# Optimization experiments

Hardware: AMD Instinct MI355X
Metric: run time of the kernel (lower is better)

Reference implementation:

```python
import math
import jax, jax.numpy as jnp
from jax import lax
import numpy as np

B, T_ENC, T_DEC = 32, 256, 800
ENC_SPK, POS_D, MAX_LEN = 896, 128, 100
N_MEL, PRE, ATT, DEC = 80, 256, 1024, 1024
IN1 = PRE + ENC_SPK + POS_D  # 1280 = first_rnn input
PROJ_IN = DEC + ENC_SPK + POS_D  # 2048


def make_pe(max_len, d):
    pe = np.zeros((max_len, d), np.float32)
    pos = np.arange(max_len, dtype=np.float32)[:, None]
    div = np.exp(np.arange(0, d, 2, dtype=np.float32) * (-math.log(10000.0) / d))
    pe[:, 0::2] = np.sin(pos * div)
    pe[:, 1::2] = np.cos(pos * div)
    return jnp.asarray(pe)


def lstm_cell(x, h, c, W_ih, W_hh, b_ih, b_hh):
    g = x @ W_ih.T + b_ih + h @ W_hh.T + b_hh
    i, f, gg, o = jnp.split(g, 4, axis=-1)  # torch LSTMCell gate order i,f,g,o
    c_new = jax.nn.sigmoid(f) * c + jax.nn.sigmoid(i) * jnp.tanh(gg)
    h_new = jax.nn.sigmoid(o) * jnp.tanh(c_new)
    return h_new, c_new


def setup_inputs() -> dict:
    key = jax.random.key(0)
    ks = jax.random.split(key, 24)
    s = 0.02  # weight init scale
    inp = {}
    inp["memory"] = jax.random.normal(ks[0], (B, T_ENC, ENC_SPK), jnp.float32)
    inp["durations_in_frames"] = jax.random.uniform(ks[1], (B, T_ENC), jnp.float32, 1.0, 7.0)
    inp["duration_frames_indices"] = jax.random.randint(ks[2], (B, T_DEC), 0, MAX_LEN)
    inp["range_pred"] = jax.random.uniform(ks[3], (B, T_ENC, 1), jnp.float32, 0.5, 2.5)
    inp["decoder_inputs"] = jax.random.normal(ks[4], (B, N_MEL, T_DEC), jnp.float32)
    inp["memory_lengths"] = jax.random.randint(ks[5], (B,), T_ENC // 2, T_ENC + 1)
    # prenet (no bias)
    inp["W_p1"] = jax.random.normal(ks[6], (PRE, N_MEL), jnp.float32) * s
    inp["W_p2"] = jax.random.normal(ks[7], (PRE, PRE), jnp.float32) * s
    # first LSTMCell
    inp["W_ih1"] = jax.random.normal(ks[8], (4 * ATT, IN1), jnp.float32) * s
    inp["W_hh1"] = jax.random.normal(ks[9], (4 * ATT, ATT), jnp.float32) * s
    inp["b_ih1"] = jnp.zeros((4 * ATT,), jnp.float32)
    inp["b_hh1"] = jnp.zeros((4 * ATT,), jnp.float32)
    # second LSTMCell
    inp["W_ih2"] = jax.random.normal(ks[10], (4 * DEC, ATT), jnp.float32) * s
    inp["W_hh2"] = jax.random.normal(ks[11], (4 * DEC, DEC), jnp.float32) * s
    inp["b_ih2"] = jnp.zeros((4 * DEC,), jnp.float32)
    inp["b_hh2"] = jnp.zeros((4 * DEC,), jnp.float32)
    # linear projection (2048 -> 80)
    inp["W_proj"] = jax.random.normal(ks[12], (N_MEL, PROJ_IN), jnp.float32) * s
    inp["b_proj"] = jnp.zeros((N_MEL,), jnp.float32)
    # deterministic prenet dropout uniforms (p=0.5, training=True always in Prenet)
    inp["u1"] = jax.random.uniform(ks[13], (T_DEC + 1, B, PRE), jnp.float32)
    inp["u2"] = jax.random.uniform(ks[14], (T_DEC + 1, B, PRE), jnp.float32)
    return inp


def reference(memory, durations_in_frames, duration_frames_indices, range_pred,
              decoder_inputs, memory_lengths,
              W_p1, W_p2, W_ih1, W_hh1, b_ih1, b_hh1,
              W_ih2, W_hh2, b_ih2, b_hh2, W_proj, b_proj, u1, u2):
    dtype = memory.dtype
    pe = make_pe(MAX_LEN, POS_D)
    # parse decoder inputs: [B, n_mel, T] -> [T, B, n_mel]; prepend go frame
    dec_in = jnp.transpose(decoder_inputs, (2, 0, 1))
    dec_in = jnp.concatenate([jnp.zeros((1, B, N_MEL), dtype), dec_in], axis=0)
    # prenet: relu->dropout(0.5) x2 (inverted dropout, scale 1/(1-p)=2)
    m1 = jnp.where(u1 >= 0.5, 2.0, 0.0).astype(dtype)
    m2 = jnp.where(u2 >= 0.5, 2.0, 0.0).astype(dtype)
    x = jax.nn.relu(dec_in @ W_p1.T) * m1
    x = jax.nn.relu(x @ W_p2.T) * m2  # [T_DEC+1, B, PRE]
    prenet_out = x[:T_DEC]
    # Gaussian upsampling constants (independent of decoder step)
    sigma = range_pred[..., 0] + 1e-05                      # [B, T_ENC]
    c_vec = jnp.cumsum(durations_in_frames, axis=1) - durations_in_frames / 2
    coef = 1.0 / jnp.sqrt(2.0 * np.pi * sigma ** 2)
    steps = jnp.arange(T_DEC, dtype=dtype)
    pos_t = duration_frames_indices.T                       # [T_DEC, B]

    def step(carry, inp):
        h1, c1, h2, c2 = carry
        x_t, t, pos = inp
        prob = coef * jnp.exp(-((t - c_vec) ** 2) / (sigma ** 2) / 2) + 1e-05
        w = prob / jnp.sum(prob, axis=1, keepdims=True)     # [B, T_ENC]
        ctx = jnp.einsum('bt,bte->be', w, memory)           # [B, ENC_SPK]
        ctx_pe = jnp.concatenate([ctx, pe[pos]], axis=-1)   # [B, ENC_SPK+POS_D]
        inp1 = jnp.concatenate([x_t, ctx_pe], axis=-1)
        h1, c1 = lstm_cell(inp1, h1, c1, W_ih1, W_hh1, b_ih1, b_hh1)
        h2, c2 = lstm_cell(h1, h2, c2, W_ih2, W_hh2, b_ih2, b_hh2)
        mel = jnp.concatenate([h2, ctx_pe], axis=1) @ W_proj.T + b_proj
        return (h1, c1, h2, c2), (mel, w)

    init = (jnp.zeros((B, ATT), dtype), jnp.zeros((B, ATT), dtype),
            jnp.zeros((B, DEC), dtype), jnp.zeros((B, DEC), dtype))
    _, (mels, ws) = lax.scan(step, init, (prenet_out, steps, pos_t))
    mel_outputs = jnp.transpose(mels, (1, 2, 0))            # [B, N_MEL, T_DEC]
    alignments = jnp.transpose(ws, (1, 0, 2))               # [B, T_DEC, T_ENC]
    return mel_outputs, alignments
```

## Files before the change

kernel.cpp:

```cpp
#include <hip/hip_runtime.h>
#include <hip/hip_bf16.h>
#include <math.h>

typedef __attribute__((ext_vector_type(8))) short bfrag8;
typedef __attribute__((ext_vector_type(4))) float f32x4;
#define AGENT __HIP_MEMORY_SCOPE_AGENT

static __device__ __forceinline__ float b2f(unsigned short u) {
  union { unsigned int i; float f; } v; v.i = ((unsigned int)u) << 16; return v.f;
}
static __device__ __forceinline__ unsigned short f2b(float f) {
  union { float f; unsigned int i; } v; v.f = f;
  unsigned int i = v.i;
  return (unsigned short)((i + 0x7FFFu + ((i >> 16) & 1u)) >> 16);
}
static __device__ __forceinline__ float sigf(float x) { return 1.f / (1.f + __expf(-x)); }


__global__ void k_init(unsigned int* hzero, unsigned int* cnt, float* pe) {
  int idx = blockIdx.x * 256 + threadIdx.x;
  if (idx < 256) cnt[idx] = 0u;
  if (idx < 65536) hzero[idx] = 0u;
  if (idx < 6400) {
    int p = idx >> 6, i = idx & 63;
// ... 74 lines not shown
  float p = coef[b * 256 + e] * __expf(-dt * dt * inv2[b * 256 + e]) + 1e-5f;
  float s = p;
#pragma unroll
  for (int o = 1; o < 64; o <<= 1) s += __shfl_xor(s, o);
  if ((e & 63) == 0) red[e >> 6] = s;
  __syncthreads();
  float tot = red[0] + red[1] + red[2] + red[3];
  out_align[((size_t)b * 800 + t) * 256 + e] = p / tot;
}

__global__ __launch_bounds__(256) void k_ctx(const float* __restrict__ cvec,
                                             const float* __restrict__ coef,
                                             const float* __restrict__ inv2,
                                             const float* __restrict__ mem,
                                             unsigned short* inp1c,
                                             int t0, int tbeg, int tend) {
  __shared__ float wl[4096];
  __shared__ float rinv[16];
  int b = blockIdx.y, tB = tbeg + blockIdx.x * 16, tid = threadIdx.x;
  int nt = tend - tB; if (nt > 16) nt = 16;
  float cv = cvec[b * 256 + tid], co = coef[b * 256 + tid], iv = inv2[b * 256 + tid];
  for (int s = 0; s < nt; ++s) {
    float d = (float)(tB + s) - cv;
    wl[s * 256 + tid] = co * __expf(-d * d * iv) + 1e-5f;
  }
  for (int s = nt; s < 16; ++s) wl[s * 256 + tid] = 0.f;
  __syncthreads();
  int wv = tid >> 6, ln = tid & 63;
  for (int s = wv; s < nt; s += 4) {
    float x = wl[s * 256 + ln] + wl[s * 256 + 64 + ln] + wl[s * 256 + 128 + ln] + wl[s * 256 + 192 + ln];
#pragma unroll
    for (int o = 1; o < 64; o <<= 1) x += __shfl_xor(x, o);
    if (ln == 0) rinv[s] = 1.f / x;
  }
  __syncthreads();
  for (int s = 0; s < nt; ++s) wl[s * 256 + tid] *= rinv[s];
  __syncthreads();
  float acc[16][4];
#pragma unroll
  for (int s = 0; s < 16; ++s) { acc[s][0] = 0.f; acc[s][1] = 0.f; acc[s][2] = 0.f; acc[s][3] = 0.f; }
  for (int e = 0; e < 256; ++e) {
    const float* mrow = mem + ((size_t)b * 256 + e) * 896;
    float m0 = mrow[tid], m1 = mrow[tid + 256], m2 = mrow[tid + 512];
    float m3 = (tid < 128) ? mrow[tid + 768] : 0.f;
#pragma unroll
    for (int s = 0; s < 16; ++s) {
      float w = wl[s * 256 + e];
      acc[s][0] += w * m0; acc[s][1] += w * m1; acc[s][2] += w * m2; acc[s][3] += w * m3;
    }
  }
  for (int s = 0; s < nt; ++s) {
    size_t base = ((size_t)(tB - t0 + s) * 32 + b) * 1280 + 256;
    inp1c[base + tid]       = f2b(acc[s][0]);
    inp1c[base + tid + 256] = f2b(acc[s][1]);
    inp1c[base + tid + 512] = f2b(acc[s][2]);
    if (tid < 128) inp1c[base + tid + 768] = f2b(acc[s][3]);
  }
}

__global__ void k_pegather(const int* __restrict__ dfi, const float* __restrict__ pe,
                           unsigned short* inp1c, int t0, int tbeg, int R) {
  int idx = blockIdx.x * 256 + threadIdx.x;
  if (idx >= R * 4096) return;
  int d = idx & 127, r = idx >> 7;
  int b = r & 31, ti = r >> 5;
  int t = tbeg + ti;
  int pos = dfi[b * 800 + t];
  inp1c[((size_t)(t - t0) * 32 + b) * 1280 + 1152 + d] = f2b(pe[pos * 128 + d]);
}

__global__ void k_repackW(const float* __restrict__ Wih1, unsigned short* wbf) {
  int idx = blockIdx.x * 256 + threadIdx.x;
  if (idx >= 1310720) return;
  float4 f = *(const float4*)(Wih1 + (size_t)idx * 4);
  union { unsigned short us[4]; unsigned long long q; } o;
  o.us[0] = f2b(f.x); o.us[1] = f2b(f.y); o.us[2] = f2b(f.z); o.us[3] = f2b(f.w);
  *(unsigned long long*)(wbf + (size_t)idx * 4) = o.q;
}

__global__ void k_repackImg(const float* __restrict__ Whh1, const float* __restrict__ Wih2,
                            const float* __restrict__ Whh2, unsigned short* wimg) {
  size_t idx = (size_t)blockIdx.x * 256 + threadIdx.x;
  if (idx >= 12582912ull) return;
  int wg = (int)(idx / 49152);
  int rem = (int)(idx % 49152);
  int gi = rem / 16384;
  int r2 = rem & 16383;
  int ks = r2 >> 9;
  int l  = (r2 >> 3) & 63;
  int e  = r2 & 7;
  int nn = l & 15, kq = l >> 4;
  int row = (nn >> 2) * 1024 + wg * 4 + (nn & 3);
  int kk = ks * 32 + kq * 8 + e;
  const float* W = (gi == 0) ? Whh1 : (gi == 1) ? Wih2 : Whh2;
  wimg[idx] = f2b(W[(size_t)row * 1024 + kk]);
}

__global__ __launch_bounds__(256) void k_melpre(const unsigned short* __restrict__ inp1c,
                                                const float* __restrict__ Wproj,
                                                const float* __restrict__ bproj,
                                                unsigned short* melpre, int t0, int tbeg) {
  extern __shared__ unsigned short ctx[];
  int t = tbeg + blockIdx.x, tid = threadIdx.x;
  int tt = t - t0;
  for (int i = tid; i < 32768; i += 256)
    ctx[i] = inp1c[((size_t)tt * 32 + (i >> 10)) * 1280 + 256 + (i & 1023)];
  __syncthreads();
  if (tid < 240) {
    int c = tid % 80, bs = tid / 80;
    const float* w = Wproj + (size_t)c * 2048 + 1024;
    for (int b = bs; b < 32; b += 3) {
      float s = bproj[c];
      const unsigned short* x = ctx + b * 1024;
#pragma unroll 8
      for (int kk = 0; kk < 1024; ++kk) s += b2f(x[kk]) * w[kk];
      melpre[((size_t)t * 32 + b) * 80 + c] = f2b(s);
    }
  }
}

#define COH_LOAD8(d0,d1,d2,d3,d4,d5,d6,d7, p0,p1,p2,p3,p4,p5,p6,p7)       \
  asm volatile(                                                            \
    "global_load_dwordx4 %0, %8, off sc0 sc1\n\t"                          \
    "global_load_dwordx4 %1, %9, off sc0 sc1\n\t"                          \
    "global_load_dwordx4 %2, %10, off sc0 sc1\n\t"                         \
    "global_load_dwordx4 %3, %11, off sc0 sc1\n\t"                         \
    "global_load_dwordx4 %4, %12, off sc0 sc1\n\t"                         \
    "global_load_dwordx4 %5, %13, off sc0 sc1\n\t"                         \
    "global_load_dwordx4 %6, %14, off sc0 sc1\n\t"                         \
    "global_load_dwordx4 %7, %15, off sc0 sc1\n\t"                         \
    "s_waitcnt vmcnt(0)"                                                   \
    : "=&v"(d0), "=&v"(d1), "=&v"(d2), "=&v"(d3),                          \
      "=&v"(d4), "=&v"(d5), "=&v"(d6), "=&v"(d7)                           \
    : "v"(p0), "v"(p1), "v"(p2), "v"(p3),                                  \
      "v"(p4), "v"(p5), "v"(p6), "v"(p7)                                   \
    : "memory")

struct DecArgs {
  const unsigned short* inp1c;
  const unsigned short* wbf;
  const unsigned short* wimg;
  const float* bih1; const float* bhh1; const float* bih2; const float* bhh2;
  const float* Wproj; const float* bproj;
  const unsigned short* melpre;
  unsigned short* h1; unsigned short* h2; float* cst;
  unsigned int* cnt; float* out_mel;
  int k0, k1;
};

__global__ __launch_bounds__(512, 1) void k_decode(DecArgs A) {
  extern __shared__ char smem[];
  float (*g1)[17]  = (float(*)[17])(smem + 131072);
  float (*g2a)[17] = (float(*)[17])(smem + 133248);
  float (*g2b)[17] = (float(*)[17])(smem + 135424);
  float (*c1)[4]   = (float(*)[4])(smem + 137600);
  float (*c2)[4]   = (float(*)[4])(smem + 138112);
  float* bias1     = (float*)(smem + 138624);
  float* bias2     = (float*)(smem + 138688);

  int wg = blockIdx.x, tid = threadIdx.x;
  int wid = tid >> 6, lane = tid & 63;
  int k0 = A.k0, k1 = A.k1;
  const unsigned short* wimg_wg = A.wimg + (size_t)wg * 49152;

  if (tid < 16) {
    int row = (tid >> 2) * 1024 + wg * 4 + (tid & 3);
    bias1[tid] = A.bih1[row] + A.bhh1[row];
    bias2[tid] = A.bih2[row] + A.bhh2[row];
  }
  if (tid < 128) {
    int b = tid >> 2, jj = tid & 3;
    c1[b][jj] = (k0 == 0) ? 0.f : A.cst[((size_t)wg * 32 + b) * 4 + jj];
  } else if (tid < 256) {
    int b = (tid - 128) >> 2, jj = tid & 3;
    c2[b][jj] = (k0 == 0) ? 0.f : A.cst[32768 + ((size_t)wg * 32 + b) * 4 + jj];
  }
  __syncthreads();

  long totspin = 0;
  for (int k = k0; k < k1; ++k) {
    bool do1 = (k < 800);
    bool do2 = (k >= 1 && k <= 800);

    {
      const char* s1 = (const char*)(A.h1 + ((k - 1) & 1) * 32768);
      const char* s2 = (const char*)(A.h2 + (k & 1) * 32768);
      ulonglong2 d0,d1,d2,d3,d4,d5,d6,d7, e0,e1,e2,e3,e4,e5,e6,e7;
      COH_LOAD8(d0,d1,d2,d3,d4,d5,d6,d7,
                s1 + ((size_t)(0*512)+tid)*16, s1 + ((size_t)(1*512)+tid)*16,
                s1 + ((size_t)(2*512)+tid)*16, s1 + ((size_t)(3*512)+tid)*16,
                s1 + ((size_t)(4*512)+tid)*16, s1 + ((size_t)(5*512)+tid)*16,
                s1 + ((size_t)(6*512)+tid)*16, s1 + ((size_t)(7*512)+tid)*16);
      COH_LOAD8(e0,e1,e2,e3,e4,e5,e6,e7,
                s2 + ((size_t)(0*512)+tid)*16, s2 + ((size_t)(1*512)+tid)*16,
                s2 + ((size_t)(2*512)+tid)*16, s2 + ((size_t)(3*512)+tid)*16,
                s2 + ((size_t)(4*512)+tid)*16, s2 + ((size_t)(5*512)+tid)*16,
                s2 + ((size_t)(6*512)+tid)*16, s2 + ((size_t)(7*512)+tid)*16);
#define STG_WR(j, va, vb)                                            \
      { int m = (j)*512 + tid;                                       \
        int sw = (m * 16) ^ (((m >> 7) & 7) << 4);                   \
        *(ulonglong2*)(smem + sw) = va;                              \
        *(ulonglong2*)(smem + 65536 + sw) = vb; }
      STG_WR(0, d0, e0); STG_WR(1, d1, e1); STG_WR(2, d2, e2); STG_WR(3, d3, e3);
      STG_WR(4, d4, e4); STG_WR(5, d5, e5); STG_WR(6, d6, e6); STG_WR(7, d7, e7);
#undef STG_WR
    }
    __syncthreads();

    if (wid < 2) {
      if (do1) {
        int nn = lane & 15, kq = lane >> 4;
        int brow = wid * 16 + nn;
        int row = (nn >> 2) * 1024 + wg * 4 + (nn & 3);
        f32x4 a0 = {0.f,0.f,0.f,0.f}, a1 = {0.f,0.f,0.f,0.f};
        size_t tt = (size_t)(k - k0 + 2);
        const unsigned short* arow = A.inp1c + (tt * 32 + brow) * 1280 + kq * 8;
        const unsigned short* wrow = A.wbf + (size_t)row * 1280 + kq * 8;
#pragma unroll 4
        for (int ks = 0; ks < 40; ks += 2) {
          bfrag8 aA = *(const bfrag8*)(arow + ks * 32);
          bfrag8 aB = *(const bfrag8*)(arow + ks * 32 + 32);
          bfrag8 b0 = *(const bfrag8*)(wrow + ks * 32);
          bfrag8 b1 = *(const bfrag8*)(wrow + ks * 32 + 32);
          a0 = __builtin_amdgcn_mfma_f32_16x16x32_bf16(aA, b0, a0, 0, 0, 0);
          a1 = __builtin_amdgcn_mfma_f32_16x16x32_bf16(aB, b1, a1, 0, 0, 0);
        }
        const bfrag8* bp = (const bfrag8*)wimg_wg + lane;
        int sbase = brow * 2048 + kq * 16;
        int sxor = (brow & 7) << 4;
#pragma unroll
        for (int ks = 0; ks < 32; ks += 2) {
          ulonglong2 v0 = *(const ulonglong2*)(smem + ((sbase + ks * 64) ^ sxor));
          ulonglong2 v1 = *(const ulonglong2*)(smem + ((sbase + (ks + 1) * 64) ^ sxor));
          union { unsigned long long q[2]; bfrag8 v; } aa, ab;
          aa.q[0] = v0.x; aa.q[1] = v0.y;
          ab.q[0] = v1.x; ab.q[1] = v1.y;
          a0 = __builtin_amdgcn_mfma_f32_16x16x32_bf16(aa.v, bp[ks * 64], a0, 0, 0, 0);
          a1 = __builtin_amdgcn_mfma_f32_16x16x32_bf16(ab.v, bp[(ks + 1) * 64], a1, 0, 0, 0);
        }
        f32x4 acc = a0 + a1;
#pragma unroll
        for (int q = 0; q < 4; ++q) g1[wid * 16 + kq * 4 + q][nn] = acc[q];
      }
    } else if (wid < 6) {
      if (do2) {
        int mt, imgbase, hoff;
        if (wid < 4) { mt = wid - 2; imgbase = 2048; hoff = 0; }
        else         { mt = wid - 4; imgbase = 4096; hoff = 65536; }
        int nn = lane & 15, kq = lane >> 4;
        int brow = mt * 16 + nn;
        f32x4 a0 = {0.f,0.f,0.f,0.f}, a1 = {0.f,0.f,0.f,0.f};
        const bfrag8* bp = (const bfrag8*)wimg_wg + imgbase + lane;
        int sbase = hoff + brow * 2048 + kq * 16;
        int sxor = (brow & 7) << 4;
#pragma unroll
        for (int ks = 0; ks < 32; ks += 2) {
          ulonglong2 v0 = *(const ulonglong2*)(smem + ((sbase + ks * 64) ^ sxor));
          ulonglong2 v1 = *(const ulonglong2*)(smem + ((sbase + (ks + 1) * 64) ^ sxor));
          union { unsigned long long q[2]; bfrag8 v; } aa, ab;
          aa.q[0] = v0.x; aa.q[1] = v0.y;
          ab.q[0] = v1.x; ab.q[1] = v1.y;
          a0 = __builtin_amdgcn_mfma_f32_16x16x32_bf16(aa.v, bp[ks * 64], a0, 0, 0, 0);
          a1 = __builtin_amdgcn_mfma_f32_16x16x32_bf16(ab.v, bp[(ks + 1) * 64], a1, 0, 0, 0);
        }
        f32x4 acc = a0 + a1;
        float (*gb)[17] = (wid < 4) ? g2a : g2b;
#pragma unroll
        for (int q = 0; q < 4; ++q) gb[mt * 16 + kq * 4 + q][nn] = acc[q];
      }
    } else {
      if (k >= 2 && wg < 80) {
        int t = k - 2;
        int L = (wid - 6) * 64 + lane;
        int b = L >> 2, q = L & 3;
        const float* wp = A.Wproj + (size_t)wg * 2048 + q * 256;
        float s0 = 0.f, s1v = 0.f;
        int sbase = 65536 + b * 2048 + q * 512;
        int sxor = (b & 7) << 4;
#pragma unroll 8
        for (int ii = 0; ii < 32; ++ii) {
          ulonglong2 v = *(const ulonglong2*)(smem + ((sbase + ii * 16) ^ sxor));
          union { unsigned long long q; unsigned short u[4]; } a_, b2_;
          a_.q = v.x; b2_.q = v.y;
          const float* w0 = wp + ii * 8;
          s0  += b2f(a_.u[0])*w0[0] + b2f(a_.u[1])*w0[1] + b2f(a_.u[2])*w0[2] + b2f(a_.u[3])*w0[3];
          s1v += b2f(b2_.u[0])*w0[4] + b2f(b2_.u[1])*w0[5] + b2f(b2_.u[2])*w0[6] + b2f(b2_.u[3])*w0[7];
        }
        float s = s0 + s1v;
        s += __shfl_xor(s, 1);
        s += __shfl_xor(s, 2);
        if (q == 0) {
          float add = b2f(A.melpre[((size_t)t * 32 + b) * 80 + wg]);
          A.out_mel[(size_t)b * 64000 + (size_t)wg * 800 + t] = s + add;
        }
      }
    }
    __syncthreads();
    if (tid < 128) {
      if (do1) {
        int b = tid >> 2, jj = tid & 3;
        float gi = g1[b][jj]      + bias1[jj];
        float gf = g1[b][4 + jj]  + bias1[4 + jj];
        float gg = g1[b][8 + jj]  + bias1[8 + jj];
        float go = g1[b][12 + jj] + bias1[12 + jj];
        float c = c1[b][jj];
        float cn = sigf(gf) * c + sigf(gi) * tanhf(gg);
        c1[b][jj] = cn;
        float hn = sigf(go) * tanhf(cn);
        float ho = __shfl_xor(hn, 1);
        if ((jj & 1) == 0) {
          unsigned int pk = (unsigned int)f2b(hn) | ((unsigned int)f2b(ho) << 16);
          __hip_atomic_store((unsigned int*)(A.h1 + (k & 1) * 32768 + b * 1024 + wg * 4 + jj), pk,
                             __ATOMIC_RELAXED, AGENT);
        }
      }
    } else if (tid < 256) {
      if (do2) {
        int b = (tid - 128) >> 2, jj = tid & 3;
        float gi = g2a[b][jj]      + g2b[b][jj]      + bias2[jj];
        float gf = g2a[b][4 + jj]  + g2b[b][4 + jj]  + bias2[4 + jj];
        float gg = g2a[b][8 + jj]  + g2b[b][8 + jj]  + bias2[8 + jj];
        float go = g2a[b][12 + jj] + g2b[b][12 + jj] + bias2[12 + jj];
        float c = c2[b][jj];
        float cn = sigf(gf) * c + sigf(gi) * tanhf(gg);
        c2[b][jj] = cn;
        float hn = sigf(go) * tanhf(cn);
        float ho = __shfl_xor(hn, 1);
        if ((jj & 1) == 0) {
          unsigned int pk = (unsigned int)f2b(hn) | ((unsigned int)f2b(ho) << 16);
          __hip_atomic_store((unsigned int*)(A.h2 + ((k - 1) & 1) * 32768 + b * 1024 + wg * 4 + jj), pk,
                             __ATOMIC_RELAXED, AGENT);
        }
      }
    }
    __syncthreads();
    if (tid == 0) {
      asm volatile("s_waitcnt vmcnt(0)" ::: "memory");
      __hip_atomic_fetch_add(A.cnt + (wg & 15) * 16, 1u, __ATOMIC_RELAXED, AGENT);
    }
    if (tid < 16 && totspin >= 0) {
      unsigned int tgt = (unsigned int)(k + 1) * 16u;
      while (__hip_atomic_load(A.cnt + tid * 16, __ATOMIC_RELAXED, AGENT) < tgt) {
        __builtin_amdgcn_s_sleep(8);
        if (++totspin > (1l << 25)) {
          totspin = -1;
          __hip_atomic_fetch_add(A.cnt + 255, 1u, __ATOMIC_RELAXED, AGENT);
          break;
        }
      }
    }
    __syncthreads();
  }
  if (tid < 128) {
    int b = tid >> 2, jj = tid & 3;
    A.cst[((size_t)wg * 32 + b) * 4 + jj] = c1[b][jj];
  } else if (tid < 256) {
    int b = (tid - 128) >> 2, jj = tid & 3;
    A.cst[32768 + ((size_t)wg * 32 + b) * 4 + jj] = c2[b][jj];
  }
}

__global__ void k_diag(float* out_mel, float wsmb) {
  out_mel[0] = 1000.f + wsmb;
}
__global__ void k_verify(const unsigned int* cnt, float* out_mel) {
  unsigned int tot = 0;
  for (int i = 0; i < 16; ++i) tot += cnt[i * 16];
  unsigned int wd = cnt[255];
  if (wd)
    out_mel[0] = 5000.f + (float)(wd > 900u ? 900u : wd);
  else if (tot != 802u * 256u)
    out_mel[0] = 3000.f + (float)tot * (1.f / 256.f);
}

extern "C" void kernel_launch(void* const* d_in, const int* in_sizes, int n_in,
                              void* d_out, int out_size, void* d_ws, size_t ws_size,
                              hipStream_t stream) {
  const float* memory = (const float*)d_in[0];
  const float* dur    = (const float*)d_in[1];
  const int*   dfi    = (const int*)d_in[2];
  const float* range  = (const float*)d_in[3];
  const float* din    = (const float*)d_in[4];
  const float* Wp1    = (const float*)d_in[6];
  const float* Wp2    = (const float*)d_in[7];
  const float* Wih1   = (const float*)d_in[8];
  const float* Whh1   = (const float*)d_in[9];
  const float* bih1   = (const float*)d_in[10];
  const float* bhh1   = (const float*)d_in[11];
  const float* Wih2   = (const float*)d_in[12];
  const float* Whh2   = (const float*)d_in[13];
  const float* bih2   = (const float*)d_in[14];
  const float* bhh2   = (const float*)d_in[15];
  const float* Wproj  = (const float*)d_in[16];
  const float* bproj  = (const float*)d_in[17];
  const float* u1     = (const float*)d_in[18];
  const float* u2     = (const float*)d_in[19];

  char* ws = (char*)d_ws;
  unsigned int* cnt   = (unsigned int*)ws;
  float* cvec         = (float*)(ws + 4096);
  float* coef         = cvec + 8192;
  float* inv2         = coef + 8192;
  float* pe           = (float*)(ws + 102400);
  unsigned short* h1  = (unsigned short*)(ws + 153600);
  unsigned short* h2  = h1 + 65536;
  float* cst          = (float*)(ws + 415744);
  unsigned short* melpre = (unsigned short*)(ws + 720896);
  unsigned short* wbf    = (unsigned short*)(ws + 4849664);
  unsigned short* wimg   = (unsigned short*)(ws + 15728640);
  unsigned short* inp1c  = (unsigned short*)(ws + 41943040ull);

  float* out_mel   = (float*)d_out;
  float* out_align = out_mel + 2048000;

  const size_t BASE = 41943040ull;
  int TC;
  if      (ws_size >= BASE + 802ull * 81920ull) TC = 800;
  else if (ws_size >= BASE + 202ull * 81920ull) TC = 200;
  else if (ws_size >= BASE +  82ull * 81920ull) TC = 80;
  else if (ws_size >= BASE +  42ull * 81920ull) TC = 40;
  else {
    k_diag<<<1, 1, 0, stream>>>(out_mel, (float)(ws_size >> 20));
    return;
  }

  hipFuncSetAttribute((const void*)k_decode, hipFuncAttributeMaxDynamicSharedMemorySize, 147456);
  hipFuncSetAttribute((const void*)k_melpre, hipFuncAttributeMaxDynamicSharedMemorySize, 98304);

  k_init<<<256, 256, 0, stream>>>((unsigned int*)(ws + 153600), cnt, pe);
  k_attn_prep<<<32, 256, 0, stream>>>(dur, range, cvec, coef, inv2);
  k_attn<<<dim3(800, 32), 256, 0, stream>>>(cvec, coef, inv2, out_align);
  k_repackW<<<5120, 256, 0, stream>>>(Wih1, wbf);
  k_repackImg<<<49152, 256, 0, stream>>>(Whh1, Wih2, Whh2, wimg);

  DecArgs da[20];
  int nch = (800 + TC - 1) / TC;
  for (int c = 0; c < nch; ++c) {
    int k0 = c * TC;
    int k1 = (c == nch - 1) ? 802 : (c + 1) * TC;
    int t0 = k0 - 2;
    int tbeg = t0 < 0 ? 0 : t0;
    int tend = k1 < 800 ? k1 : 800;
    int R = tend - tbeg;
    k_prenet<<<R, 256, 0, stream>>>(din, u1, u2, Wp1, Wp2, inp1c, t0, tbeg);
    k_ctx<<<dim3((R + 15) / 16, 32), 256, 0, stream>>>(cvec, coef, inv2, memory, inp1c, t0, tbeg, tend);
    k_pegather<<<(R * 4096 + 255) / 256, 256, 0, stream>>>(dfi, pe, inp1c, t0, tbeg, R);
    k_melpre<<<R, 256, 65536, stream>>>(inp1c, Wproj, bproj, melpre, t0, tbeg);

    da[c] = DecArgs{ inp1c, wbf, wimg, bih1, bhh1, bih2, bhh2,
                     Wproj, bproj, melpre, h1, h2, cst, cnt, out_mel, k0, k1 };
    void* kp[1] = { &da[c] };
    hipLaunchCooperativeKernel((const void*)k_decode, dim3(256), dim3(512), kp, 139264, stream);
  }
  k_verify<<<1, 1, 0, stream>>>(cnt, out_mel);
}
```

Before: 22.17 ms.

## Shrink persistent decoder grid to 64 workgroups and prefetch input GEMM during barrier

The persistent cooperative LSTM decoder is repartitioned from 256 workgroups owning 4 hidden units each to 64 workgroups owning 16 units each. The weight image is repacked to match, and the gate GEMM now uses all four gates per wave. The input-to-hidden GEMM for the next step (which does not depend on h) is computed while waiting on the grid barrier, moving it off the critical path. Fewer workgroups make the per-step global barrier cheaper, at the cost of more MFMA and weight traffic per workgroup. The projection work is redistributed over 40 workgroups and the watchdog diagnostics are simplified.

```diff
diff --git a/kernel.cpp b/kernel.cpp
--- a/kernel.cpp
+++ b/kernel.cpp
@@ -180,17 +180,19 @@
                             const float* __restrict__ Whh2, unsigned short* wimg) {
   size_t idx = (size_t)blockIdx.x * 256 + threadIdx.x;
   if (idx >= 12582912ull) return;
-  int wg = (int)(idx / 49152);
-  int rem = (int)(idx % 49152);
-  int gi = rem / 16384;
-  int r2 = rem & 16383;
-  int ks = r2 >> 9;
-  int l  = (r2 >> 3) & 63;
-  int e  = r2 & 7;
+  int wg  = (int)(idx / 196608);
+  int r   = (int)(idx % 196608);
+  int mat = r / 65536;
+  int r2  = r % 65536;
+  int g   = r2 >> 14;
+  int r3  = r2 & 16383;
+  int ks  = r3 >> 9;
+  int l   = (r3 >> 3) & 63;
+  int e   = r3 & 7;
   int nn = l & 15, kq = l >> 4;
-  int row = (nn >> 2) * 1024 + wg * 4 + (nn & 3);
+  int row = g * 1024 + wg * 16 + nn;
   int kk = ks * 32 + kq * 8 + e;
-  const float* W = (gi == 0) ? Whh1 : (gi == 1) ? Wih2 : Whh2;
+  const float* W = (mat == 0) ? Whh1 : (mat == 1) ? Wih2 : Whh2;
   wimg[idx] = f2b(W[(size_t)row * 1024 + kk]);
 }
 
@@ -234,12 +236,47 @@
       "v"(p4), "v"(p5), "v"(p6), "v"(p7)                                   \
     : "memory")
 
+#define XGEMM(kn, gg_)                                                                \
+  { xa0 = (f32x4){0.f,0.f,0.f,0.f}; xa1 = (f32x4){0.f,0.f,0.f,0.f};                   \
+    int nn_ = lane & 15, kq_ = lane >> 4;                                             \
+    int row_ = (gg_) * 1024 + wg * 16 + nn_;                                          \
+    size_t tt_ = (size_t)((kn) - k0 + 2);                                             \
+    const unsigned short* a0_ = A.inp1c + (tt_ * 32 + nn_) * 1280 + kq_ * 8;          \
+    const unsigned short* a1_ = A.inp1c + (tt_ * 32 + 16 + nn_) * 1280 + kq_ * 8;     \
+    const unsigned short* w_  = A.wbf + (size_t)row_ * 1280 + kq_ * 8;                \
+    _Pragma("unroll 4")                                                               \
+    for (int ks_ = 0; ks_ < 40; ++ks_) {                                              \
+      bfrag8 bA_ = *(const bfrag8*)(w_ + ks_ * 32);                                   \
+      bfrag8 aA_ = *(const bfrag8*)(a0_ + ks_ * 32);                                  \
+      bfrag8 aB_ = *(const bfrag8*)(a1_ + ks_ * 32);                                  \
+      xa0 = __builtin_amdgcn_mfma_f32_16x16x32_bf16(aA_, bA_, xa0, 0, 0, 0);          \
+      xa1 = __builtin_amdgcn_mfma_f32_16x16x32_bf16(aB_, bA_, xa1, 0, 0, 0);          \
+    } }
+
+#define HMFMA(hoff, bp)                                                               \
+  { int nn_ = lane & 15, kq_ = lane >> 4;                                             \
+    int sb0 = (hoff) + nn_ * 2048 + kq_ * 16;                                         \
+    int sb1 = (hoff) + (16 + nn_) * 2048 + kq_ * 16;                                  \
+    int sx0 = (nn_ & 7) << 4;                                                         \
+    int sx1 = ((16 + nn_) & 7) << 4;                                                  \
+    _Pragma("unroll")                                                                 \
+    for (int ks_ = 0; ks_ < 32; ++ks_) {                                              \
+      bfrag8 bb_ = (bp)[ks_ * 64];                                                    \
+      ulonglong2 v0_ = *(const ulonglong2*)(smem + ((sb0 + ks_ * 64) ^ sx0));         \
+      ulonglong2 v1_ = *(const ulonglong2*)(smem + ((sb1 + ks_ * 64) ^ sx1));         \
+      union { unsigned long long q[2]; bfrag8 v; } ua_, ub_;                          \
+      ua_.q[0] = v0_.x; ua_.q[1] = v0_.y;                                             \
+      ub_.q[0] = v1_.x; ub_.q[1] = v1_.y;                                             \
+      a0 = __builtin_amdgcn_mfma_f32_16x16x32_bf16(ua_.v, bb_, a0, 0, 0, 0);          \
+      a1 = __builtin_amdgcn_mfma_f32_16x16x32_bf16(ub_.v, bb_, a1, 0, 0, 0);          \
+    } }
+
 struct DecArgs {
   const unsigned short* inp1c;
   const unsigned short* wbf;
   const unsigned short* wimg;
   const float* bih1; const float* bhh1; const float* bih2; const float* bhh2;
-  const float* Wproj; const float* bproj;
+  const float* Wproj;
   const unsigned short* melpre;
   unsigned short* h1; unsigned short* h2; float* cst;
   unsigned int* cnt; float* out_mel;
@@ -248,32 +285,33 @@
 
 __global__ __launch_bounds__(512, 1) void k_decode(DecArgs A) {
   extern __shared__ char smem[];
-  float (*g1)[17]  = (float(*)[17])(smem + 131072);
-  float (*g2a)[17] = (float(*)[17])(smem + 133248);
-  float (*g2b)[17] = (float(*)[17])(smem + 135424);
-  float (*c1)[4]   = (float(*)[4])(smem + 137600);
-  float (*c2)[4]   = (float(*)[4])(smem + 138112);
-  float* bias1     = (float*)(smem + 138624);
-  float* bias2     = (float*)(smem + 138688);
+  float* g1f   = (float*)(smem + 131072);
+  float* g2f   = (float*)(smem + 139776);
+  float* c1    = (float*)(smem + 148480);
+  float* c2    = (float*)(smem + 150528);
+  float* bias1 = (float*)(smem + 152576);
+  float* bias2 = (float*)(smem + 152832);
 
   int wg = blockIdx.x, tid = threadIdx.x;
   int wid = tid >> 6, lane = tid & 63;
   int k0 = A.k0, k1 = A.k1;
-  const unsigned short* wimg_wg = A.wimg + (size_t)wg * 49152;
-
-  if (tid < 16) {
-    int row = (tid >> 2) * 1024 + wg * 4 + (tid & 3);
+  const unsigned short* wimg_wg = A.wimg + (size_t)wg * 196608;
+
+  if (tid < 64) {
+    int g = tid >> 4, jj = tid & 15;
+    int row = g * 1024 + wg * 16 + jj;
     bias1[tid] = A.bih1[row] + A.bhh1[row];
     bias2[tid] = A.bih2[row] + A.bhh2[row];
   }
-  if (tid < 128) {
-    int b = tid >> 2, jj = tid & 3;
-    c1[b][jj] = (k0 == 0) ? 0.f : A.cst[((size_t)wg * 32 + b) * 4 + jj];
-  } else if (tid < 256) {
-    int b = (tid - 128) >> 2, jj = tid & 3;
-    c2[b][jj] = (k0 == 0) ? 0.f : A.cst[32768 + ((size_t)wg * 32 + b) * 4 + jj];
-  }
-  __syncthreads();
+  {
+    int b = tid >> 4, jj = tid & 15;
+    c1[b * 16 + jj] = (k0 == 0) ? 0.f : A.cst[((size_t)wg * 32 + b) * 16 + jj];
+    c2[b * 16 + jj] = (k0 == 0) ? 0.f : A.cst[32768 + ((size_t)wg * 32 + b) * 16 + jj];
+  }
+  __syncthreads();
+
+  f32x4 xa0 = {0.f,0.f,0.f,0.f}, xa1 = {0.f,0.f,0.f,0.f};
+  if (wid < 4 && k0 < 800) XGEMM(k0, wid);
 
   long totspin = 0;
   for (int k = k0; k < k1; ++k) {
@@ -281,19 +319,15 @@
     bool do2 = (k >= 1 && k <= 800);
 
     {
-      const char* s1 = (const char*)(A.h1 + ((k - 1) & 1) * 32768);
-      const char* s2 = (const char*)(A.h2 + (k & 1) * 32768);
+      const char* s1g = (const char*)(A.h1 + ((k - 1) & 1) * 32768);
+      const char* s2g = (const char*)(A.h2 + (k & 1) * 32768);
+      const char* p1 = s1g + tid * 16;
+      const char* p2 = s2g + tid * 16;
       ulonglong2 d0,d1,d2,d3,d4,d5,d6,d7, e0,e1,e2,e3,e4,e5,e6,e7;
       COH_LOAD8(d0,d1,d2,d3,d4,d5,d6,d7,
-                s1 + ((size_t)(0*512)+tid)*16, s1 + ((size_t)(1*512)+tid)*16,
-                s1 + ((size_t)(2*512)+tid)*16, s1 + ((size_t)(3*512)+tid)*16,
-                s1 + ((size_t)(4*512)+tid)*16, s1 + ((size_t)(5*512)+tid)*16,
-                s1 + ((size_t)(6*512)+tid)*16, s1 + ((size_t)(7*512)+tid)*16);
+                p1, p1+8192, p1+16384, p1+24576, p1+32768, p1+40960, p1+49152, p1+57344);
       COH_LOAD8(e0,e1,e2,e3,e4,e5,e6,e7,
-                s2 + ((size_t)(0*512)+tid)*16, s2 + ((size_t)(1*512)+tid)*16,
-                s2 + ((size_t)(2*512)+tid)*16, s2 + ((size_t)(3*512)+tid)*16,
-                s2 + ((size_t)(4*512)+tid)*16, s2 + ((size_t)(5*512)+tid)*16,
-                s2 + ((size_t)(6*512)+tid)*16, s2 + ((size_t)(7*512)+tid)*16);
+                p2, p2+8192, p2+16384, p2+24576, p2+32768, p2+40960, p2+49152, p2+57344);
 #define STG_WR(j, va, vb)                                            \
       { int m = (j)*512 + tid;                                       \
         int sw = (m * 16) ^ (((m >> 7) & 7) << 4);                   \
@@ -305,73 +339,24 @@
     }
     __syncthreads();
 
-    if (wid < 2) {
+    if (wid < 4) {
+      int g = wid;
       if (do1) {
+        f32x4 a0 = xa0, a1 = xa1;
+        const bfrag8* bp = (const bfrag8*)(wimg_wg) + g * 2048 + lane;
+        HMFMA(0, bp);
         int nn = lane & 15, kq = lane >> 4;
-        int brow = wid * 16 + nn;
-        int row = (nn >> 2) * 1024 + wg * 4 + (nn & 3);
-        f32x4 a0 = {0.f,0.f,0.f,0.f}, a1 = {0.f,0.f,0.f,0.f};
-        size_t tt = (size_t)(k - k0 + 2);
-        const unsigned short* arow = A.inp1c + (tt * 32 + brow) * 1280 + kq * 8;
-        const unsigned short* wrow = A.wbf + (size_t)row * 1280 + kq * 8;
-#pragma unroll 4
-        for (int ks = 0; ks < 40; ks += 2) {
-          bfrag8 aA = *(const bfrag8*)(arow + ks * 32);
-          bfrag8 aB = *(const bfrag8*)(arow + ks * 32 + 32);
-          bfrag8 b0 = *(const bfrag8*)(wrow + ks * 32);
-          bfrag8 b1 = *(const bfrag8*)(wrow + ks * 32 + 32);
-          a0 = __builtin_amdgcn_mfma_f32_16x16x32_bf16(aA, b0, a0, 0, 0, 0);
-          a1 = __builtin_amdgcn_mfma_f32_16x16x32_bf16(aB, b1, a1, 0, 0, 0);
-        }
-        const bfrag8* bp = (const bfrag8*)wimg_wg + lane;
-        int sbase = brow * 2048 + kq * 16;
-        int sxor = (brow & 7) << 4;
 #pragma unroll
-        for (int ks = 0; ks < 32; ks += 2) {
-          ulonglong2 v0 = *(const ulonglong2*)(smem + ((sbase + ks * 64) ^ sxor));
-          ulonglong2 v1 = *(const ulonglong2*)(smem + ((sbase + (ks + 1) * 64) ^ sxor));
-          union { unsigned long long q[2]; bfrag8 v; } aa, ab;
-          aa.q[0] = v0.x; aa.q[1] = v0.y;
-          ab.q[0] = v1.x; ab.q[1] = v1.y;
-          a0 = __builtin_amdgcn_mfma_f32_16x16x32_bf16(aa.v, bp[ks * 64], a0, 0, 0, 0);
-          a1 = __builtin_amdgcn_mfma_f32_16x16x32_bf16(ab.v, bp[(ks + 1) * 64], a1, 0, 0, 0);
-        }
-        f32x4 acc = a0 + a1;
-#pragma unroll
-        for (int q = 0; q < 4; ++q) g1[wid * 16 + kq * 4 + q][nn] = acc[q];
+        for (int q = 0; q < 4; ++q) {
+          g1f[(kq * 4 + q) * 68 + g * 16 + nn]        = a0[q];
+          g1f[(16 + kq * 4 + q) * 68 + g * 16 + nn]   = a1[q];
+        }
       }
-    } else if (wid < 6) {
-      if (do2) {
-        int mt, imgbase, hoff;
-        if (wid < 4) { mt = wid - 2; imgbase = 2048; hoff = 0; }
-        else         { mt = wid - 4; imgbase = 4096; hoff = 65536; }
-        int nn = lane & 15, kq = lane >> 4;
-        int brow = mt * 16 + nn;
-        f32x4 a0 = {0.f,0.f,0.f,0.f}, a1 = {0.f,0.f,0.f,0.f};
-        const bfrag8* bp = (const bfrag8*)wimg_wg + imgbase + lane;
-        int sbase = hoff + brow * 2048 + kq * 16;
-        int sxor = (brow & 7) << 4;
-#pragma unroll
-        for (int ks = 0; ks < 32; ks += 2) {
-          ulonglong2 v0 = *(const ulonglong2*)(smem + ((sbase + ks * 64) ^ sxor));
-          ulonglong2 v1 = *(const ulonglong2*)(smem + ((sbase + (ks + 1) * 64) ^ sxor));
-          union { unsigned long long q[2]; bfrag8 v; } aa, ab;
-          aa.q[0] = v0.x; aa.q[1] = v0.y;
-          ab.q[0] = v1.x; ab.q[1] = v1.y;
-          a0 = __builtin_amdgcn_mfma_f32_16x16x32_bf16(aa.v, bp[ks * 64], a0, 0, 0, 0);
-          a1 = __builtin_amdgcn_mfma_f32_16x16x32_bf16(ab.v, bp[(ks + 1) * 64], a1, 0, 0, 0);
-        }
-        f32x4 acc = a0 + a1;
-        float (*gb)[17] = (wid < 4) ? g2a : g2b;
-#pragma unroll
-        for (int q = 0; q < 4; ++q) gb[mt * 16 + kq * 4 + q][nn] = acc[q];
-      }
-    } else {
-      if (k >= 2 && wg < 80) {
+      if (k >= 2 && wg < 40 && tid < 256) {
         int t = k - 2;
-        int L = (wid - 6) * 64 + lane;
-        int b = L >> 2, q = L & 3;
-        const float* wp = A.Wproj + (size_t)wg * 2048 + q * 256;
+        int dot = tid >> 2, q = tid & 3;
+        int col = 2 * wg + (dot >> 5), b = dot & 31;
+        const float* wp = A.Wproj + (size_t)col * 2048 + q * 256;
         float s0 = 0.f, s1v = 0.f;
         int sbase = 65536 + b * 2048 + q * 512;
         int sxor = (b & 7) << 4;
@@ -388,45 +373,59 @@
         s += __shfl_xor(s, 1);
         s += __shfl_xor(s, 2);
         if (q == 0) {
-          float add = b2f(A.melpre[((size_t)t * 32 + b) * 80 + wg]);
-          A.out_mel[(size_t)b * 64000 + (size_t)wg * 800 + t] = s + add;
+          float add = b2f(A.melpre[((size_t)t * 32 + b) * 80 + col]);
+          A.out_mel[(size_t)b * 64000 + (size_t)col * 800 + t] = s + add;
         }
       }
+    } else {
+      int g = wid - 4;
+      if (do2) {
+        f32x4 a0 = {0.f,0.f,0.f,0.f}, a1 = {0.f,0.f,0.f,0.f};
+        const bfrag8* bpA = (const bfrag8*)(wimg_wg) + 8192 + g * 2048 + lane;
+        HMFMA(0, bpA);
+        const bfrag8* bpB = (const bfrag8*)(wimg_wg) + 16384 + g * 2048 + lane;
+        HMFMA(65536, bpB);
+        int nn = lane & 15, kq = lane >> 4;
+#pragma unroll
+        for (int q = 0; q < 4; ++q) {
+          g2f[(kq * 4 + q) * 68 + g * 16 + nn]        = a0[q];
+          g2f[(16 + kq * 4 + q) * 68 + g * 16 + nn]   = a1[q];
+        }
+      }
     }
     __syncthreads();
-    if (tid < 128) {
+
+    {
+      int b = tid >> 4, jj = tid & 15;
       if (do1) {
-        int b = tid >> 2, jj = tid & 3;
-        float gi = g1[b][jj]      + bias1[jj];
-        float gf = g1[b][4 + jj]  + bias1[4 + jj];
-        float gg = g1[b][8 + jj]  + bias1[8 + jj];
-        float go = g1[b][12 + jj] + bias1[12 + jj];
-        float c = c1[b][jj];
+        float gi = g1f[b * 68 + jj]      + bias1[jj];
+        float gf = g1f[b * 68 + 16 + jj] + bias1[16 + jj];
+        float gg = g1f[b * 68 + 32 + jj] + bias1[32 + jj];
+        float go = g1f[b * 68 + 48 + jj] + bias1[48 + jj];
+        float c = c1[b * 16 + jj];
         float cn = sigf(gf) * c + sigf(gi) * tanhf(gg);
-        c1[b][jj] = cn;
+        c1[b * 16 + jj] = cn;
         float hn = sigf(go) * tanhf(cn);
         float ho = __shfl_xor(hn, 1);
         if ((jj & 1) == 0) {
           unsigned int pk = (unsigned int)f2b(hn) | ((unsigned int)f2b(ho) << 16);
-          __hip_atomic_store((unsigned int*)(A.h1 + (k & 1) * 32768 + b * 1024 + wg * 4 + jj), pk,
+          __hip_atomic_store((unsigned int*)(A.h1 + (k & 1) * 32768 + b * 1024 + wg * 16 + jj), pk,
                              __ATOMIC_RELAXED, AGENT);
         }
       }
-    } else if (tid < 256) {
       if (do2) {
-        int b = (tid - 128) >> 2, jj = tid & 3;
-        float gi = g2a[b][jj]      + g2b[b][jj]      + bias2[jj];
-        float gf = g2a[b][4 + jj]  + g2b[b][4 + jj]  + bias2[4 + jj];
-        float gg = g2a[b][8 + jj]  + g2b[b][8 + jj]  + bias2[8 + jj];
-        float go = g2a[b][12 + jj] + g2b[b][12 + jj] + bias2[12 + jj];
-        float c = c2[b][jj];
+        float gi = g2f[b * 68 + jj]      + bias2[jj];
+        float gf = g2f[b * 68 + 16 + jj] + bias2[16 + jj];
+        float gg = g2f[b * 68 + 32 + jj] + bias2[32 + jj];
+        float go = g2f[b * 68 + 48 + jj] + bias2[48 + jj];
+        float c = c2[b * 16 + jj];
         float cn = sigf(gf) * c + sigf(gi) * tanhf(gg);
-        c2[b][jj] = cn;
+        c2[b * 16 + jj] = cn;
         float hn = sigf(go) * tanhf(cn);
         float ho = __shfl_xor(hn, 1);
         if ((jj & 1) == 0) {
           unsigned int pk = (unsigned int)f2b(hn) | ((unsigned int)f2b(ho) << 16);
-          __hip_atomic_store((unsigned int*)(A.h2 + ((k - 1) & 1) * 32768 + b * 1024 + wg * 4 + jj), pk,
+          __hip_atomic_store((unsigned int*)(A.h2 + ((k - 1) & 1) * 32768 + b * 1024 + wg * 16 + jj), pk,
                              __ATOMIC_RELAXED, AGENT);
         }
       }
@@ -434,13 +433,18 @@
     __syncthreads();
     if (tid == 0) {
       asm volatile("s_waitcnt vmcnt(0)" ::: "memory");
-      __hip_atomic_fetch_add(A.cnt + (wg & 15) * 16, 1u, __ATOMIC_RELAXED, AGENT);
-    }
-    if (tid < 16 && totspin >= 0) {
-      unsigned int tgt = (unsigned int)(k + 1) * 16u;
-      while (__hip_atomic_load(A.cnt + tid * 16, __ATOMIC_RELAXED, AGENT) < tgt) {
+      __hip_atomic_fetch_add(A.cnt + (wg & 7) * 16, 1u, __ATOMIC_RELAXED, AGENT);
+    }
+    if (wid < 4) {
+      int kn = k + 1;
+      if (kn < k1 && kn < 800) XGEMM(kn, wid);
+    }
+    if (tid >= 448 && tid < 456 && totspin >= 0) {
+      int li = tid - 448;
+      unsigned int tgt = (unsigned int)(k + 1) * 8u;
+      while (__hip_atomic_load(A.cnt + li * 16, __ATOMIC_RELAXED, AGENT) < tgt) {
         __builtin_amdgcn_s_sleep(8);
-        if (++totspin > (1l << 25)) {
+        if (++totspin > (1l << 23)) {
           totspin = -1;
           __hip_atomic_fetch_add(A.cnt + 255, 1u, __ATOMIC_RELAXED, AGENT);
           break;
@@ -449,12 +453,10 @@
     }
     __syncthreads();
   }
-  if (tid < 128) {
-    int b = tid >> 2, jj = tid & 3;
-    A.cst[((size_t)wg * 32 + b) * 4 + jj] = c1[b][jj];
-  } else if (tid < 256) {
-    int b = (tid - 128) >> 2, jj = tid & 3;
-    A.cst[32768 + ((size_t)wg * 32 + b) * 4 + jj] = c2[b][jj];
+  {
+    int b = tid >> 4, jj = tid & 15;
+    A.cst[((size_t)wg * 32 + b) * 16 + jj] = c1[b * 16 + jj];
+    A.cst[32768 + ((size_t)wg * 32 + b) * 16 + jj] = c2[b * 16 + jj];
   }
 }
 
@@ -463,12 +465,9 @@
 }
 __global__ void k_verify(const unsigned int* cnt, float* out_mel) {
   unsigned int tot = 0;
-  for (int i = 0; i < 16; ++i) tot += cnt[i * 16];
-  unsigned int wd = cnt[255];
-  if (wd)
-    out_mel[0] = 5000.f + (float)(wd > 900u ? 900u : wd);
-  else if (tot != 802u * 256u)
-    out_mel[0] = 3000.f + (float)tot * (1.f / 256.f);
+  for (int i = 0; i < 8; ++i) tot += cnt[i * 16];
+  if (tot != 802u * 64u)
+    out_mel[0] = 3000.f + (float)tot * (1.f / 64.f);
 }
 
 extern "C" void kernel_launch(void* const* d_in, const int* in_sizes, int n_in,
@@ -522,7 +521,7 @@
     return;
   }
 
-  hipFuncSetAttribute((const void*)k_decode, hipFuncAttributeMaxDynamicSharedMemorySize, 147456);
+  hipFuncSetAttribute((const void*)k_decode, hipFuncAttributeMaxDynamicSharedMemorySize, 153088);
   hipFuncSetAttribute((const void*)k_melpre, hipFuncAttributeMaxDynamicSharedMemorySize, 98304);
 
   k_init<<<256, 256, 0, stream>>>((unsigned int*)(ws + 153600), cnt, pe);
@@ -546,9 +545,9 @@
     k_melpre<<<R, 256, 65536, stream>>>(inp1c, Wproj, bproj, melpre, t0, tbeg);
 
     da[c] = DecArgs{ inp1c, wbf, wimg, bih1, bhh1, bih2, bhh2,
-                     Wproj, bproj, melpre, h1, h2, cst, cnt, out_mel, k0, k1 };
+                     Wproj, melpre, h1, h2, cst, cnt, out_mel, k0, k1 };
     void* kp[1] = { &da[c] };
-    hipLaunchCooperativeKernel((const void*)k_decode, dim3(256), dim3(512), kp, 139264, stream);
+    hipLaunchCooperativeKernel((const void*)k_decode, dim3(64), dim3(512), kp, 153088, stream);
   }
   k_verify<<<1, 1, 0, stream>>>(cnt, out_mel);
 }
```

After: 39.94 ms. +80.1%, slower.

## Prefetch next step's input GEMM during grid barrier and reorder hidden-state layout

Applied to the files above, without the earlier changes.

The input-projection MFMA for LSTM1, which does not depend on the recurrence, now runs for step k+1 while the barrier spin for step k is in progress. Its accumulators carry over into the next iteration, taking that GEMM off the per-step critical path. The global h1/h2 buffers switch to a workgroup-major layout ([wg][b][4]), so each workgroup's stores are contiguous, and the LDS staging scatter is rewritten to match. Spinning moves to threads in waves other than the prefetching waves, and the watchdog limit shrinks. Costs are extra registers held across the barrier and scattered 8-byte LDS writes.

```diff
diff --git a/kernel.cpp b/kernel.cpp
--- a/kernel.cpp
+++ b/kernel.cpp
@@ -234,12 +234,44 @@
       "v"(p4), "v"(p5), "v"(p6), "v"(p7)                                   \
     : "memory")
 
+#define XGEMM(kn)                                                                     \
+  { xa0 = (f32x4){0.f,0.f,0.f,0.f}; xa1 = (f32x4){0.f,0.f,0.f,0.f};                   \
+    int nn_ = lane & 15, kq_ = lane >> 4;                                             \
+    int brow_ = wid * 16 + nn_;                                                       \
+    int row_ = (nn_ >> 2) * 1024 + wg * 4 + (nn_ & 3);                                \
+    size_t tt_ = (size_t)((kn) - k0 + 2);                                             \
+    const unsigned short* arow_ = A.inp1c + (tt_ * 32 + brow_) * 1280 + kq_ * 8;      \
+    const unsigned short* wrow_ = A.wbf + (size_t)row_ * 1280 + kq_ * 8;              \
+    _Pragma("unroll 4")                                                               \
+    for (int ks_ = 0; ks_ < 40; ks_ += 2) {                                           \
+      bfrag8 aA_ = *(const bfrag8*)(arow_ + ks_ * 32);                                \
+      bfrag8 aB_ = *(const bfrag8*)(arow_ + ks_ * 32 + 32);                           \
+      bfrag8 b0_ = *(const bfrag8*)(wrow_ + ks_ * 32);                                \
+      bfrag8 b1_ = *(const bfrag8*)(wrow_ + ks_ * 32 + 32);                           \
+      xa0 = __builtin_amdgcn_mfma_f32_16x16x32_bf16(aA_, b0_, xa0, 0, 0, 0);          \
+      xa1 = __builtin_amdgcn_mfma_f32_16x16x32_bf16(aB_, b1_, xa1, 0, 0, 0);          \
+    } }
+
+#define HMFMA_LDS(hoff, bp, brow)                                                     \
+  { int kq_ = lane >> 4;                                                              \
+    int sb_ = (hoff) + (brow) * 2048 + kq_ * 16;                                      \
+    int sx_ = ((brow) & 7) << 4;                                                      \
+    _Pragma("unroll")                                                                 \
+    for (int ks_ = 0; ks_ < 32; ks_ += 2) {                                           \
+      ulonglong2 v0_ = *(const ulonglong2*)(smem + ((sb_ + ks_ * 64) ^ sx_));         \
+      ulonglong2 v1_ = *(const ulonglong2*)(smem + ((sb_ + (ks_ + 1) * 64) ^ sx_));   \
+      union { unsigned long long q[2]; bfrag8 v; } ua_, ub_;                          \
+      ua_.q[0] = v0_.x; ua_.q[1] = v0_.y;                                             \
+      ub_.q[0] = v1_.x; ub_.q[1] = v1_.y;                                             \
+      a0 = __builtin_amdgcn_mfma_f32_16x16x32_bf16(ua_.v, (bp)[ks_ * 64], a0, 0, 0, 0); \
+      a1 = __builtin_amdgcn_mfma_f32_16x16x32_bf16(ub_.v, (bp)[(ks_ + 1) * 64], a1, 0, 0, 0); } }
+
 struct DecArgs {
   const unsigned short* inp1c;
   const unsigned short* wbf;
   const unsigned short* wimg;
   const float* bih1; const float* bhh1; const float* bih2; const float* bhh2;
-  const float* Wproj; const float* bproj;
+  const float* Wproj;
   const unsigned short* melpre;
   unsigned short* h1; unsigned short* h2; float* cst;
   unsigned int* cnt; float* out_mel;
@@ -275,30 +307,34 @@
   }
   __syncthreads();
 
+  f32x4 xa0 = {0.f,0.f,0.f,0.f}, xa1 = {0.f,0.f,0.f,0.f};
+  if (wid < 2 && k0 < 800) XGEMM(k0);
+
   long totspin = 0;
   for (int k = k0; k < k1; ++k) {
     bool do1 = (k < 800);
     bool do2 = (k >= 1 && k <= 800);
 
     {
-      const char* s1 = (const char*)(A.h1 + ((k - 1) & 1) * 32768);
-      const char* s2 = (const char*)(A.h2 + (k & 1) * 32768);
+      const char* s1g = (const char*)(A.h1 + ((k - 1) & 1) * 32768);
+      const char* s2g = (const char*)(A.h2 + (k & 1) * 32768);
+      const char* p1 = s1g + tid * 16;
+      const char* p2 = s2g + tid * 16;
       ulonglong2 d0,d1,d2,d3,d4,d5,d6,d7, e0,e1,e2,e3,e4,e5,e6,e7;
       COH_LOAD8(d0,d1,d2,d3,d4,d5,d6,d7,
-                s1 + ((size_t)(0*512)+tid)*16, s1 + ((size_t)(1*512)+tid)*16,
-                s1 + ((size_t)(2*512)+tid)*16, s1 + ((size_t)(3*512)+tid)*16,
-                s1 + ((size_t)(4*512)+tid)*16, s1 + ((size_t)(5*512)+tid)*16,
-                s1 + ((size_t)(6*512)+tid)*16, s1 + ((size_t)(7*512)+tid)*16);
+                p1, p1+8192, p1+16384, p1+24576, p1+32768, p1+40960, p1+49152, p1+57344);
       COH_LOAD8(e0,e1,e2,e3,e4,e5,e6,e7,
-                s2 + ((size_t)(0*512)+tid)*16, s2 + ((size_t)(1*512)+tid)*16,
-                s2 + ((size_t)(2*512)+tid)*16, s2 + ((size_t)(3*512)+tid)*16,
-                s2 + ((size_t)(4*512)+tid)*16, s2 + ((size_t)(5*512)+tid)*16,
-                s2 + ((size_t)(6*512)+tid)*16, s2 + ((size_t)(7*512)+tid)*16);
-#define STG_WR(j, va, vb)                                            \
-      { int m = (j)*512 + tid;                                       \
-        int sw = (m * 16) ^ (((m >> 7) & 7) << 4);                   \
-        *(ulonglong2*)(smem + sw) = va;                              \
-        *(ulonglong2*)(smem + 65536 + sw) = vb; }
+                p2, p2+8192, p2+16384, p2+24576, p2+32768, p2+40960, p2+49152, p2+57344);
+#define STG_WR(j, va, vb)                                                          \
+      { int m = (j)*512 + tid;                                                     \
+        int wgs = m >> 4;                                                          \
+        int b0 = (m & 15) * 2;                                                     \
+        int a0_ = (b0 * 2048 + wgs * 8)       ^ ((b0 & 7) << 4);                   \
+        int a1_ = ((b0 + 1) * 2048 + wgs * 8) ^ (((b0 + 1) & 7) << 4);             \
+        *(unsigned long long*)(smem + a0_)         = va.x;                         \
+        *(unsigned long long*)(smem + a1_)         = va.y;                         \
+        *(unsigned long long*)(smem + 65536 + a0_) = vb.x;                         \
+        *(unsigned long long*)(smem + 65536 + a1_) = vb.y; }
       STG_WR(0, d0, e0); STG_WR(1, d1, e1); STG_WR(2, d2, e2); STG_WR(3, d3, e3);
       STG_WR(4, d4, e4); STG_WR(5, d5, e5); STG_WR(6, d6, e6); STG_WR(7, d7, e7);
 #undef STG_WR
@@ -307,64 +343,38 @@
 
     if (wid < 2) {
       if (do1) {
-        int nn = lane & 15, kq = lane >> 4;
+        int nn = lane & 15;
         int brow = wid * 16 + nn;
-        int row = (nn >> 2) * 1024 + wg * 4 + (nn & 3);
+        f32x4 a0 = xa0, a1 = xa1;
+        const bfrag8* bp = (const bfrag8*)wimg_wg + lane;
+        HMFMA_LDS(0, bp, brow);
+        int kq = lane >> 4;
+#pragma unroll
+        for (int q = 0; q < 4; ++q) g1[wid * 16 + kq * 4 + q][nn] = (a0 + a1)[q];
+      }
+    } else if (wid < 4) {
+      if (do2) {
+        int mt = wid - 2;
+        int nn = lane & 15;
+        int brow = mt * 16 + nn;
         f32x4 a0 = {0.f,0.f,0.f,0.f}, a1 = {0.f,0.f,0.f,0.f};
-        size_t tt = (size_t)(k - k0 + 2);
-        const unsigned short* arow = A.inp1c + (tt * 32 + brow) * 1280 + kq * 8;
-        const unsigned short* wrow = A.wbf + (size_t)row * 1280 + kq * 8;
-#pragma unroll 4
-        for (int ks = 0; ks < 40; ks += 2) {
-          bfrag8 aA = *(const bfrag8*)(arow + ks * 32);
-          bfrag8 aB = *(const bfrag8*)(arow + ks * 32 + 32);
-          bfrag8 b0 = *(const bfrag8*)(wrow + ks * 32);
-          bfrag8 b1 = *(const bfrag8*)(wrow + ks * 32 + 32);
-          a0 = __builtin_amdgcn_mfma_f32_16x16x32_bf16(aA, b0, a0, 0, 0, 0);
-          a1 = __builtin_amdgcn_mfma_f32_16x16x32_bf16(aB, b1, a1, 0, 0, 0);
-        }
-        const bfrag8* bp = (const bfrag8*)wimg_wg + lane;
-        int sbase = brow * 2048 + kq * 16;
-        int sxor = (brow & 7) << 4;
-#pragma unroll
-        for (int ks = 0; ks < 32; ks += 2) {
-          ulonglong2 v0 = *(const ulonglong2*)(smem + ((sbase + ks * 64) ^ sxor));
-          ulonglong2 v1 = *(const ulonglong2*)(smem + ((sbase + (ks + 1) * 64) ^ sxor));
-          union { unsigned long long q[2]; bfrag8 v; } aa, ab;
-          aa.q[0] = v0.x; aa.q[1] = v0.y;
-          ab.q[0] = v1.x; ab.q[1] = v1.y;
-          a0 = __builtin_amdgcn_mfma_f32_16x16x32_bf16(aa.v, bp[ks * 64], a0, 0, 0, 0);
-          a1 = __builtin_amdgcn_mfma_f32_16x16x32_bf16(ab.v, bp[(ks + 1) * 64], a1, 0, 0, 0);
-        }
-        f32x4 acc = a0 + a1;
-#pragma unroll
-        for (int q = 0; q < 4; ++q) g1[wid * 16 + kq * 4 + q][nn] = acc[q];
+        const bfrag8* bp = (const bfrag8*)wimg_wg + 2048 + lane;
+        HMFMA_LDS(0, bp, brow);
+        int kq = lane >> 4;
+#pragma unroll
+        for (int q = 0; q < 4; ++q) g2a[mt * 16 + kq * 4 + q][nn] = (a0 + a1)[q];
       }
     } else if (wid < 6) {
       if (do2) {
-        int mt, imgbase, hoff;
-        if (wid < 4) { mt = wid - 2; imgbase = 2048; hoff = 0; }
-        else         { mt = wid - 4; imgbase = 4096; hoff = 65536; }
-        int nn = lane & 15, kq = lane >> 4;
+        int mt = wid - 4;
+        int nn = lane & 15;
         int brow = mt * 16 + nn;
         f32x4 a0 = {0.f,0.f,0.f,0.f}, a1 = {0.f,0.f,0.f,0.f};
-        const bfrag8* bp = (const bfrag8*)wimg_wg + imgbase + lane;
-        int sbase = hoff + brow * 2048 + kq * 16;
-        int sxor = (brow & 7) << 4;
-#pragma unroll
-        for (int ks = 0; ks < 32; ks += 2) {
-          ulonglong2 v0 = *(const ulonglong2*)(smem + ((sbase + ks * 64) ^ sxor));
-          ulonglong2 v1 = *(const ulonglong2*)(smem + ((sbase + (ks + 1) * 64) ^ sxor));
-          union { unsigned long long q[2]; bfrag8 v; } aa, ab;
-          aa.q[0] = v0.x; aa.q[1] = v0.y;
-          ab.q[0] = v1.x; ab.q[1] = v1.y;
-          a0 = __builtin_amdgcn_mfma_f32_16x16x32_bf16(aa.v, bp[ks * 64], a0, 0, 0, 0);
-          a1 = __builtin_amdgcn_mfma_f32_16x16x32_bf16(ab.v, bp[(ks + 1) * 64], a1, 0, 0, 0);
-        }
-        f32x4 acc = a0 + a1;
-        float (*gb)[17] = (wid < 4) ? g2a : g2b;
-#pragma unroll
-        for (int q = 0; q < 4; ++q) gb[mt * 16 + kq * 4 + q][nn] = acc[q];
+        const bfrag8* bp = (const bfrag8*)wimg_wg + 4096 + lane;
+        HMFMA_LDS(65536, bp, brow);
+        int kq = lane >> 4;
+#pragma unroll
+        for (int q = 0; q < 4; ++q) g2b[mt * 16 + kq * 4 + q][nn] = (a0 + a1)[q];
       }
     } else {
       if (k >= 2 && wg < 80) {
@@ -408,7 +418,7 @@
         float ho = __shfl_xor(hn, 1);
         if ((jj & 1) == 0) {
           unsigned int pk = (unsigned int)f2b(hn) | ((unsigned int)f2b(ho) << 16);
-          __hip_atomic_store((unsigned int*)(A.h1 + (k & 1) * 32768 + b * 1024 + wg * 4 + jj), pk,
+          __hip_atomic_store((unsigned int*)(A.h1 + (k & 1) * 32768 + wg * 128 + b * 4 + jj), pk,
                              __ATOMIC_RELAXED, AGENT);
         }
       }
@@ -426,7 +436,7 @@
         float ho = __shfl_xor(hn, 1);
         if ((jj & 1) == 0) {
           unsigned int pk = (unsigned int)f2b(hn) | ((unsigned int)f2b(ho) << 16);
-          __hip_atomic_store((unsigned int*)(A.h2 + ((k - 1) & 1) * 32768 + b * 1024 + wg * 4 + jj), pk,
+          __hip_atomic_store((unsigned int*)(A.h2 + ((k - 1) & 1) * 32768 + wg * 128 + b * 4 + jj), pk,
                              __ATOMIC_RELAXED, AGENT);
         }
       }
@@ -436,11 +446,16 @@
       asm volatile("s_waitcnt vmcnt(0)" ::: "memory");
       __hip_atomic_fetch_add(A.cnt + (wg & 15) * 16, 1u, __ATOMIC_RELAXED, AGENT);
     }
-    if (tid < 16 && totspin >= 0) {
+    if (wid < 2) {
+      int kn = k + 1;
+      if (kn < k1 && kn < 800) XGEMM(kn);
+    }
+    if (tid >= 256 && tid < 272 && totspin >= 0) {
+      int li = tid - 256;
       unsigned int tgt = (unsigned int)(k + 1) * 16u;
-      while (__hip_atomic_load(A.cnt + tid * 16, __ATOMIC_RELAXED, AGENT) < tgt) {
+      while (__hip_atomic_load(A.cnt + li * 16, __ATOMIC_RELAXED, AGENT) < tgt) {
         __builtin_amdgcn_s_sleep(8);
-        if (++totspin > (1l << 25)) {
+        if (++totspin > (1l << 23)) {
           totspin = -1;
           __hip_atomic_fetch_add(A.cnt + 255, 1u, __ATOMIC_RELAXED, AGENT);
           break;
@@ -464,10 +479,7 @@
 __global__ void k_verify(const unsigned int* cnt, float* out_mel) {
   unsigned int tot = 0;
   for (int i = 0; i < 16; ++i) tot += cnt[i * 16];
-  unsigned int wd = cnt[255];
-  if (wd)
-    out_mel[0] = 5000.f + (float)(wd > 900u ? 900u : wd);
-  else if (tot != 802u * 256u)
+  if (tot != 802u * 256u)
     out_mel[0] = 3000.f + (float)tot * (1.f / 256.f);
 }
 
@@ -546,7 +558,7 @@
     k_melpre<<<R, 256, 65536, stream>>>(inp1c, Wproj, bproj, melpre, t0, tbeg);
 
     da[c] = DecArgs{ inp1c, wbf, wimg, bih1, bhh1, bih2, bhh2,
-                     Wproj, bproj, melpre, h1, h2, cst, cnt, out_mel, k0, k1 };
+                     Wproj, melpre, h1, h2, cst, cnt, out_mel, k0, k1 };
     void* kp[1] = { &da[c] };
     hipLaunchCooperativeKernel((const void*)k_decode, dim3(256), dim3(512), kp, 139264, stream);
   }
```

New measurement: 27.02 ms. 1.22x slower.
